# Performance work log

Measured on AMD Instinct MI355X. Metric: run time of the kernel, lower is better.

## Reference

```python
import jax, jax.numpy as jnp
import numpy as np
from jax import lax

A_NUM = 3
STRIDES = (4, 8, 16, 32, 64)
LEVEL_HW = ((128, 208), (64, 104), (32, 52), (16, 26), (8, 13))
IMG_H, IMG_W = 512.0, 832.0
PRE_NMS, POST_NMS, NMS_TH = 6000, 1000, 0.7


def _base_anchors(base_size, ratios=(0.5, 1.0, 2.0), scales=(8.0,)):
    ratios = np.asarray(ratios, np.float64)
    scales = np.asarray(scales, np.float64)
    cx = cy = (base_size - 1) / 2.0
    size = float(base_size) * float(base_size)
    ws = np.round(np.sqrt(size / ratios))
    hs = np.round(ws * ratios)
    ws = (ws[:, None] * scales[None, :]).reshape(-1)
    hs = (hs[:, None] * scales[None, :]).reshape(-1)
    return np.stack([cx - 0.5 * (ws - 1), cy - 0.5 * (hs - 1),
                     cx + 0.5 * (ws - 1), cy + 0.5 * (hs - 1)], axis=1)


def _all_anchors():
    # generate_anchors_global: per-level shifted grids, concatenated, order (h, w, a)
    out = []
    for stride, (h, w) in zip(STRIDES, LEVEL_HW):
        base = _base_anchors(stride)  # [A,4]
        sx = np.arange(w) * stride
        sy = np.arange(h) * stride
        sx, sy = np.meshgrid(sx, sy)
        shifts = np.stack([sx.ravel(), sy.ravel(), sx.ravel(), sy.ravel()], axis=1)
        anc = (shifts[:, None, :] + base[None, :, :]).reshape(-1, 4)  # [H*W*A,4]
        out.append(anc)
    return np.concatenate(out, axis=0).astype(np.float32)

_ANCHORS = _all_anchors()


def _conv(x, w, b, pad):
    y = lax.conv_general_dilated(x, w, (1, 1), [(pad, pad), (pad, pad)],
                                 dimension_numbers=('NCHW', 'OIHW', 'NCHW'))
    return y + b[None, :, None, None]


def _bbox_transform_inv(anchors, deltas):
    w = anchors[:, 2] - anchors[:, 0] + 1.0
    h = anchors[:, 3] - anchors[:, 1] + 1.0
    cx = anchors[:, 0] + 0.5 * w
    cy = anchors[:, 1] + 0.5 * h
    dx, dy, dw, dh = deltas[:, 0], deltas[:, 1], deltas[:, 2], deltas[:, 3]
    pcx = dx * w + cx
    pcy = dy * h + cy
    pw = jnp.exp(dw) * w
    ph = jnp.exp(dh) * h
    return jnp.stack([pcx - 0.5 * pw, pcy - 0.5 * ph,
                      pcx + 0.5 * pw, pcy + 0.5 * ph], axis=1)


def _iou_one_to_many(box, boxes):
    area = (boxes[:, 2] - boxes[:, 0] + 1.0) * (boxes[:, 3] - boxes[:, 1] + 1.0)
    area_b = (box[2] - box[0] + 1.0) * (box[3] - box[1] + 1.0)
    xx1 = jnp.maximum(box[0], boxes[:, 0])
    yy1 = jnp.maximum(box[1], boxes[:, 1])
    xx2 = jnp.minimum(box[2], boxes[:, 2])
    yy2 = jnp.minimum(box[3], boxes[:, 3])
    iw = jnp.maximum(0.0, xx2 - xx1 + 1.0)
    ih = jnp.maximum(0.0, yy2 - yy1 + 1.0)
    inter = iw * ih
    return inter / (area + area_b - inter)


def _nms_fixed(boxes, scores, thresh, max_out):
    # greedy NMS with a fixed number of iterations (jit-friendly)
    def body(s, _):
        i = jnp.argmax(s)
        valid = s[i] > -jnp.inf
        ious = _iou_one_to_many(boxes[i], boxes)
        s2 = jnp.where(ious > thresh, -jnp.inf, s)
        s2 = s2.at[i].set(-jnp.inf)
        return s2, (i, valid)
    _, (idx, valid) = lax.scan(body, scores, None, length=max_out)
    return idx, valid


def _rpn_forward(feats, im_info, rpn_conv_w, rpn_conv_b, rpn_score_w,
                 rpn_score_b, rpn_bbox_w, rpn_bbox_b):
    fg_scores, bbox_deltas = [], []
    for p in feats:
        H, W = p.shape[-2], p.shape[-1]
        f = _conv(p, rpn_conv_w, rpn_conv_b, 1)              # [1,512,H,W]
        cls = _conv(f, rpn_score_w, rpn_score_b, 0)          # [1,2A,H,W]
        # _reshape_layer(.,2) + softmax(dim=1) + _reshape_layer back + permute
        prob = jax.nn.softmax(cls.reshape(1, 2, A_NUM, H, W), axis=1)
        prob = prob.reshape(1, 2 * A_NUM, H, W).transpose(0, 2, 3, 1)  # [1,H,W,2A]
        fg = prob[..., A_NUM:].reshape(-1)                    # fg prob, order (h,w,a)
        bb = _conv(f, rpn_bbox_w, rpn_bbox_b, 0).transpose(0, 2, 3, 1).reshape(-1, 4)
        fg_scores.append(fg)
        bbox_deltas.append(bb)
    scores = jnp.concatenate(fg_scores, axis=0)              # [Ntot]
    deltas = jnp.concatenate(bbox_deltas, axis=0)            # [Ntot,4]
    anchors = jnp.asarray(_ANCHORS)

    proposals = _bbox_transform_inv(anchors, deltas)
    # clip to image
    proposals = jnp.stack([
        jnp.clip(proposals[:, 0], 0.0, im_info[1] - 1.0),
        jnp.clip(proposals[:, 1], 0.0, im_info[0] - 1.0),
        jnp.clip(proposals[:, 2], 0.0, im_info[1] - 1.0),
        jnp.clip(proposals[:, 3], 0.0, im_info[0] - 1.0)], axis=1)

    # pre-NMS top-k by score
    top_scores, order = lax.top_k(scores, PRE_NMS)
    top_boxes = proposals[order]
    keep, valid = _nms_fixed(top_boxes, top_scores, NMS_TH, POST_NMS)
    vmask = valid.astype(top_boxes.dtype)[:, None]
    sel_boxes = top_boxes[keep] * vmask
    sel_scores = top_scores[keep][:, None] * vmask
    rois = jnp.concatenate([jnp.zeros((POST_NMS, 1), sel_boxes.dtype), sel_boxes], axis=1)
    return jnp.concatenate([rois, sel_scores], axis=1)        # [POST_NMS, 6]


def setup_inputs() -> dict:
    key = jax.random.key(0)
    ks = jax.random.split(key, 12)
    chans = 256
    feats = {}
    for i, (name, (h, w)) in enumerate(zip(['p2', 'p3', 'p4', 'p5', 'p6'], LEVEL_HW)):
        feats[name] = jax.random.normal(ks[i], (1, chans, h, w), jnp.float32)
    inp = dict(feats)
    inp['im_info'] = jnp.array([IMG_H, IMG_W, 1.0], jnp.float32)
    inp['rpn_conv_w'] = jax.random.normal(ks[5], (512, chans, 3, 3), jnp.float32) * 0.03
    inp['rpn_conv_b'] = jnp.zeros((512,), jnp.float32)
    inp['rpn_score_w'] = jax.random.normal(ks[6], (2 * A_NUM, 512, 1, 1), jnp.float32) * 0.03
    inp['rpn_score_b'] = jnp.zeros((2 * A_NUM,), jnp.float32)
    inp['rpn_bbox_w'] = jax.random.normal(ks[7], (4 * A_NUM, 512, 1, 1), jnp.float32) * 0.01
    inp['rpn_bbox_b'] = jnp.zeros((4 * A_NUM,), jnp.float32)
    return inp


def reference(p2, p3, p4, p5, p6, im_info, rpn_conv_w, rpn_conv_b,
              rpn_score_w, rpn_score_b, rpn_bbox_w, rpn_bbox_b):
    return _rpn_forward([p2, p3, p4, p5, p6], im_info, rpn_conv_w, rpn_conv_b,
                        rpn_score_w, rpn_score_b, rpn_bbox_w, rpn_bbox_b)
```

## Files before the change

kernel.cpp:

```cpp
#include <hip/hip_runtime.h>
#include <stdint.h>

#define N_ANCH   106392
#define PRE_NMS  6000
#define POST_NMS 1000
#define POOL_CAP 8192
#define NMS_BLKS 94
#define SUP_W    96

static __device__ const int    LV_H[5]      = {128, 64, 32, 16, 8};
static __device__ const int    LV_W[5]      = {208, 104, 52, 26, 13};
static __device__ const int    LV_STRIDE[5] = {4, 8, 16, 32, 64};
static __device__ const int    LV_PIX[5]    = {26624, 6656, 1664, 416, 104};
static __device__ const int    LV_TILE0[6]  = {0, 416, 520, 546, 553, 555};
static __device__ const int    LV_AOFF[6]   = {0, 79872, 99840, 104832, 106080, 106392};
static __device__ const int    GPOFF[6]     = {0, 26624, 33280, 34944, 35360, 35464};
static __device__ const double BASE_ANCH[5][3][4] = {
  {{-22.,-10.,25.,13.},   {-14.,-14.,17.,17.},    {-10.,-22.,13.,25.}},
  {{-40.,-20.,47.,27.},   {-28.,-28.,35.,35.},    {-20.,-44.,27.,51.}},
  {{-84.,-40.,99.,55.},   {-56.,-56.,71.,71.},    {-36.,-80.,51.,95.}},
  {{-164.,-72.,195.,103.},{-112.,-112.,143.,143.},{-76.,-168.,107.,199.}},
  {{-332.,-152.,395.,215.},{-224.,-224.,287.,287.},{-148.,-328.,211.,391.}}
};

__device__ __forceinline__ uint32_t sort32f(float f) {
  uint32_t u = __float_as_uint(f);
  return ((int)u < 0) ? ~u : (u | 0x80000000u);
}
__device__ __forceinline__ uint64_t sort64(double d) {
  uint64_t u = (uint64_t)__double_as_longlong(d);
  return ((long long)u < 0) ? ~u : (u | 0x8000000000000000ull);
}

__device__ __forceinline__ double combf(const float* sw, const float* bw, int c, int j) {
  if (j < 3) return (double)sw[(3 + j) * 512 + c] - (double)sw[j * 512 + c];
  return (double)bw[(j - 3) * 512 + c];
}

__global__ __launch_bounds__(256) void k_weff_part(const float* __restrict__ cw,
                                                   const float* __restrict__ sw,
                                                   const float* __restrict__ bw,
                                                   double* __restrict__ Wpart) {
  int chunk = blockIdx.x / 9;
  int tb = blockIdx.x % 9;
  int t = tb * 256 + threadIdx.x;
  int c0 = chunk * 32;
  double acc[15];
#pragma unroll
  for (int j = 0; j < 15; ++j) acc[j] = 0.0;
#pragma unroll 1
  for (int c = c0; c < c0 + 32; ++c) {
    double v = (double)cw[c * 2304 + t];
#pragma unroll
    for (int j = 0; j < 15; ++j) acc[j] += v * combf(sw, bw, c, j);
  }
  double* o = Wpart + (((size_t)chunk * 2304 + t) << 4);
#pragma unroll
  for (int j = 0; j < 15; ++j) o[j] = acc[j];
  o[15] = 0.0;
}

__global__ __launch_bounds__(256) void k_weff_fin(const double* __restrict__ Wpart,
                                                  const float* __restrict__ cb,
                                                  const float* __restrict__ sb,
                                                  const float* __restrict__ bb,
                                                  const float* __restrict__ sw,
                                                  const float* __restrict__ bw,
                                                  double* __restrict__ Weff,
                                                  double* __restrict__ fb,
                                                  float4* __restrict__ w3,
                                                  float* __restrict__ fb32) {
  if (blockIdx.x == 9) {
    __shared__ double ps[15][16];
    int tid = threadIdx.x;
    if (tid < 240) {
      int j = tid >> 4, part = tid & 15;
      double s = 0.0;
      for (int c = part * 32; c < part * 32 + 32; ++c)
        s += (double)cb[c] * combf(sw, bw, c, j);
      ps[j][part] = s;
    }
    __syncthreads();
    if (tid < 15) {
      double s = 0.0;
#pragma unroll
      for (int part = 0; part < 16; ++part) s += ps[tid][part];
      s += (tid < 3) ? ((double)sb[3 + tid] - (double)sb[tid]) : (double)bb[tid - 3];
      fb[tid] = s;
      if (tid < 3) fb32[tid] = (float)s;
    }
    if (tid == 15) fb32[3] = 0.f;
    return;
  }
  int t = blockIdx.x * 256 + threadIdx.x;
  double acc[15];
#pragma unroll
  for (int j = 0; j < 15; ++j) acc[j] = 0.0;
#pragma unroll 1
  for (int chunk = 0; chunk < 16; ++chunk) {
    const double* p = Wpart + (((size_t)chunk * 2304 + t) << 4);
#pragma unroll
    for (int j = 0; j < 15; ++j) acc[j] += p[j];
  }
  double* o = Weff + ((size_t)t << 4);
#pragma unroll
  for (int j = 0; j < 15; ++j) o[j] = acc[j];
  o[15] = 0.0;
  float4 wf;
  wf.x = (float)acc[0]; wf.y = (float)acc[1]; wf.z = (float)acc[2]; wf.w = 0.f;
  w3[t] = wf;
}

__global__ __launch_bounds__(256) void k_w5(const double* __restrict__ Weff,
                                            double* __restrict__ w5) {
  int idx = blockIdx.x * 256 + threadIdx.x;
  if (idx >= 2304 * 3) return;
  int t = idx / 3, a = idx % 3;
  int ci = t / 9, t9 = t % 9;
  const double* src = Weff + ((size_t)t << 4);
  double* dst = w5 + (size_t)ci * 192 + (size_t)(t9 * 3 + a) * 6;
  int jd = 3 + 4 * a;
  dst[0] = src[jd + 0];
  dst[1] = src[jd + 1];
  dst[2] = src[jd + 2];
  dst[3] = src[jd + 3];
  dst[4] = src[a];
  dst[5] = 0.0;
}

__device__ __forceinline__ void load9(float v[9], const float* __restrict__ ib,
                                      const bool rok[3], const bool cok[3],
                                      const int roff[3]) {
#pragma unroll
  for (int ky = 0; ky < 3; ++ky)
#pragma unroll
    for (int kx = 0; kx < 3; ++kx)
      v[ky * 3 + kx] = (rok[ky] && cok[kx]) ? ib[roff[ky] + kx] : 0.0f;
}

__global__ __launch_bounds__(256) void k_fast(
    const float* __restrict__ p0, const float* __restrict__ p1,
    const float* __restrict__ p2, const float* __restrict__ p3,
    const float* __restrict__ p4,
    const float4* __restrict__ w3, const float* __restrict__ fb32,
    float* __restrict__ logits32, uint32_t* __restrict__ hist) {
  __shared__ float4 w3s[2304];
  __shared__ float red[4][64][3];
  int tid = threadIdx.x, wv = tid >> 6, ln = tid & 63;
  for (int i = tid; i < 2304; i += 256) w3s[i] = w3[i];
  int t = blockIdx.x;
  int L = 0;
  while (L < 4 && t >= LV_TILE0[L + 1]) ++L;
  const float* inL = (L == 0) ? p0 : (L == 1) ? p1 : (L == 2) ? p2 : (L == 3) ? p3 : p4;
  int H = LV_H[L], W = LV_W[L], HW = H * W, PIX = LV_PIX[L];
  int pix = (t - LV_TILE0[L]) * 64 + ln;
  bool valid = pix < PIX;
  if (!valid) pix = PIX - 1;
  int h = pix / W, w = pix % W;
  bool rok[3], cok[3];
  int roff[3];
#pragma unroll
  for (int ky = 0; ky < 3; ++ky) {
    int iy = h + ky - 1;
    rok[ky] = (iy >= 0 && iy < H);
    roff[ky] = iy * W + w - 1;
  }
#pragma unroll
  for (int kx = 0; kx < 3; ++kx) {
    int ix = w + kx - 1;
    cok[kx] = (ix >= 0 && ix < W);
  }
  __syncthreads();
  float a0 = 0.f, a1 = 0.f, a2 = 0.f;
  int ci0 = wv * 64;
  const float* ib = inL + ci0 * HW;
#pragma unroll 1
  for (int ci = ci0; ci < ci0 + 64; ++ci, ib += HW) {
    float v[9];
    load9(v, ib, rok, cok, roff);
    const float4* wr = w3s + ci * 9;
#pragma unroll
    for (int t9 = 0; t9 < 9; ++t9) {
      float4 wt = wr[t9];
      float vv = v[t9];
      a0 += vv * wt.x; a1 += vv * wt.y; a2 += vv * wt.z;
    }
  }
  red[wv][ln][0] = a0; red[wv][ln][1] = a1; red[wv][ln][2] = a2;
  __syncthreads();
  if (wv == 0 && valid) {
    int gbase = LV_AOFF[L] + pix * 3;
#pragma unroll
    for (int a = 0; a < 3; ++a) {
      float f = (red[0][ln][a] + red[1][ln][a]) + (red[2][ln][a] + red[3][ln][a]);
      f += fb32[a];
      logits32[gbase + a] = f;
      atomicAdd(&hist[sort32f(f) >> 16], 1u);
    }
  }
}

__global__ __launch_bounds__(1024) void k_edge(const uint32_t* __restrict__ hist,
                                               uint32_t* __restrict__ cnts) {
  __shared__ uint32_t cs[1024];
  __shared__ uint32_t g_grp, g_suf;
  int t = threadIdx.x, wv = t >> 6, ln = t & 63;
#pragma unroll 4
  for (int r = 0; r < 64; ++r) {
    int g = r * 16 + wv;
    uint32_t x = hist[g * 64 + ln];
#pragma unroll
    for (int off = 32; off > 0; off >>= 1) x += __shfl_down(x, off);
    if (ln == 0) cs[g] = x;
  }
  __syncthreads();
  for (int off = 1; off < 1024; off <<= 1) {
    uint32_t v = cs[t] + ((t + off < 1024) ? cs[t + off] : 0u);
    __syncthreads();
    cs[t] = v;
    __syncthreads();
  }
  uint32_t sufnext = (t < 1023) ? cs[t + 1] : 0u;
  if (cs[t] >= PRE_NMS && sufnext < PRE_NMS) {
    g_grp = (uint32_t)t;
    g_suf = sufnext;
  }
  __syncthreads();
  if (t < 64) {
    uint32_t grp = g_grp, suf = g_suf;
    uint32_t x = hist[grp * 64 + t];
    uint32_t S = x;
#pragma unroll
    for (int off = 1; off < 64; off <<= 1) {
      uint32_t y = __shfl_down(S, off);
      if (t + off < 64) S += y;
    }
    unsigned long long mask = __ballot(suf + S >= PRE_NMS);
    int hi = 63 - (int)__clzll(mask);
    if (t == hi) {
      uint32_t e = grp * 64 + (uint32_t)hi;
      cnts[1] = (e > 2) ? e - 2 : 0;
    }
  }
}

__global__ __launch_bounds__(256) void k_cnt(const float* __restrict__ logits32,
                                             const uint32_t* __restrict__ cnts,
                                             uint32_t* __restrict__ bcnt) {
  __shared__ uint32_t wc[4];
  int tid = threadIdx.x;
  int i = blockIdx.x * 256 + tid;
  uint32_t edge = cnts[1];
  bool pass = (i < N_ANCH) && ((sort32f(logits32[i]) >> 16) >= edge);
  unsigned long long m = __ballot(pass);
  if ((tid & 63) == 0) wc[tid >> 6] = (uint32_t)__popcll(m);
  __syncthreads();
  if (tid == 0) bcnt[blockIdx.x] = wc[0] + wc[1] + wc[2] + wc[3];
}

__global__ __launch_bounds__(256) void k_fill(const float* __restrict__ logits32,
                                              uint32_t* __restrict__ cnts,
                                              const uint32_t* __restrict__ bcnt,
                                              uint32_t* __restrict__ alist) {
  __shared__ uint32_t red[256];
  __shared__ uint32_t woff[4];
  int tid = threadIdx.x, wv = tid >> 6, ln = tid & 63;
  uint32_t s = 0;
  for (int k = tid; k < blockIdx.x; k += 256) s += bcnt[k];
  red[tid] = s;
  __syncthreads();
#pragma unroll
  for (int off = 128; off > 0; off >>= 1) {
    if (tid < off) red[tid] += red[tid + off];
    __syncthreads();
  }
  uint32_t base = red[0];
  int i = blockIdx.x * 256 + tid;
  uint32_t edge = cnts[1];
  bool pass = (i < N_ANCH) && ((sort32f(logits32[i]) >> 16) >= edge);
  unsigned long long m = __ballot(pass);
  if (ln == 0) woff[wv] = (uint32_t)__popcll(m);
  __syncthreads();
  uint32_t off_in_blk = 0;
  for (int k = 0; k < wv; ++k) off_in_blk += woff[k];
  if (pass) {
    uint32_t pos = base + off_in_blk + (uint32_t)__popcll(m & ((1ull << ln) - 1ull));
    if (pos < POOL_CAP) alist[pos] = (uint32_t)i;
  }
  if (blockIdx.x == ((N_ANCH + 255) / 256 - 1) && tid == 0)
    cnts[0] = base + woff[0] + woff[1] + woff[2] + woff[3];
}

__global__ __launch_bounds__(256) void k_refine(
    const float* __restrict__ p0, const float* __restrict__ p1,
    const float* __restrict__ p2, const float* __restrict__ p3,
    const float* __restrict__ p4,
    const double* __restrict__ w5, const double* __restrict__ fb,
    const uint32_t* __restrict__ alist, const uint32_t* __restrict__ cnts,
    double* __restrict__ logits, double* __restrict__ deltas,
    uint64_t* __restrict__ pkey) {
  __shared__ int4 wlds[4][768];
  __shared__ double red[4][64][5];
  int tid = threadIdx.x, wv = tid >> 6, ln = tid & 63;
  int cnt = (int)cnts[0];
  if (cnt > POOL_CAP) cnt = POOL_CAP;
  int base = blockIdx.x * 64;
  if (base >= cnt) return;
  int slot = base + ln;
  if (slot >= cnt) slot = cnt - 1;
  int gi = (int)alist[slot];
  int gpix = gi / 3, a = gi - gpix * 3;
  int L = 0;
  while (L < 4 && gpix >= GPOFF[L + 1]) ++L;
  int pix = gpix - GPOFF[L];
  const float* inL = (L == 0) ? p0 : (L == 1) ? p1 : (L == 2) ? p2 : (L == 3) ? p3 : p4;
  int H = LV_H[L], W = LV_W[L], HW = H * W;
  int h = pix / W, w = pix % W;
  bool rok[3], cok[3];
  int roff[3];
#pragma unroll
  for (int ky = 0; ky < 3; ++ky) {
    int iy = h + ky - 1;
    rok[ky] = (iy >= 0 && iy < H);
    roff[ky] = iy * W + w - 1;
  }
#pragma unroll
  for (int kx = 0; kx < 3; ++kx) {
    int ix = w + kx - 1;
    cok[kx] = (ix >= 0 && ix < W);
  }
  const char* wbc = (const char*)&wlds[wv][0];
  {
    const int4* gs = (const int4*)((const char*)w5 + (size_t)(wv * 64) * 1536);
    int4 r[12];
#pragma unroll
    for (int i = 0; i < 12; ++i) r[i] = gs[i * 64 + ln];
#pragma unroll
    for (int i = 0; i < 12; ++i) wlds[wv][i * 64 + ln] = r[i];
  }
  double sc = 0.0, d0 = 0.0, d1 = 0.0, d2 = 0.0, d3 = 0.0;
  const float* ibn = inL + (size_t)(wv * 64) * HW;
  float vn[9];
  load9(vn, ibn, rok, cok, roff);
#pragma unroll 1
  for (int k = 0; k < 8; ++k) {
    int4 r[12];
    if (k < 7) {
      const int4* gs =
          (const int4*)((const char*)w5 + (size_t)(wv * 64 + (k + 1) * 8) * 1536);
#pragma unroll
      for (int i = 0; i < 12; ++i) r[i] = gs[i * 64 + ln];
    }
#pragma unroll 1
    for (int c2 = 0; c2 < 8; ++c2) {
      float vc[9];
#pragma unroll
      for (int q = 0; q < 9; ++q) vc[q] = vn[q];
      int lc = k * 8 + c2;
      if (lc < 63) {
        ibn += HW;
        load9(vn, ibn, rok, cok, roff);
      }
      const char* b2 = wbc + c2 * 1536 + a * 48;
#pragma unroll
      for (int t9 = 0; t9 < 9; ++t9) {
        double vd = (double)vc[t9];
        double2 w01 = *(const double2*)(b2 + t9 * 144);
        double2 w23 = *(const double2*)(b2 + t9 * 144 + 16);
        double  w4  = *(const double*)(b2 + t9 * 144 + 32);
        d0 += vd * w01.x; d1 += vd * w01.y;
        d2 += vd * w23.x; d3 += vd * w23.y;
        sc += vd * w4;
      }
    }
    if (k < 7) {
#pragma unroll
      for (int i = 0; i < 12; ++i) wlds[wv][i * 64 + ln] = r[i];
    }
  }
  red[wv][ln][0] = sc;
  red[wv][ln][1] = d0; red[wv][ln][2] = d1;
  red[wv][ln][3] = d2; red[wv][ln][4] = d3;
  __syncthreads();
  if (wv == 0) {
    int js = a, jd = 3 + 4 * a;
    double f[5];
#pragma unroll
    for (int j = 0; j < 5; ++j)
      f[j] = red[0][ln][j] + red[1][ln][j] + red[2][ln][j] + red[3][ln][j];
    double lg = f[0] + fb[js];
    logits[gi] = lg;
    deltas[gi * 4 + 0] = f[1] + fb[jd + 0];
    deltas[gi * 4 + 1] = f[2] + fb[jd + 1];
    deltas[gi * 4 + 2] = f[3] + fb[jd + 2];
    deltas[gi * 4 + 3] = f[4] + fb[jd + 3];
    pkey[slot] = (sort64(lg) & ~0x1FFFFull) | (uint64_t)(0x1FFFFu - (uint32_t)gi);
  }
}

__global__ __launch_bounds__(256) void k_rank_cnt(const uint32_t* __restrict__ cnts,
                                                  const uint64_t* __restrict__ pkey,
                                                  uint32_t* __restrict__ rank32) {
  __shared__ uint64_t lk[512];
  int t = threadIdx.x;
  int cnt = (int)cnts[0];
  if (cnt > POOL_CAP) cnt = POOL_CAP;
  int it = blockIdx.x >> 4, jc = blockIdx.x & 15;
  int e = it * 256 + t;
  int c0 = jc * 512;
  if (it * 256 >= cnt || c0 >= cnt) return;
  int lim = cnt - c0; if (lim > 512) lim = 512;
  for (int i = t; i < 512; i += 256) lk[i] = (i < lim) ? pkey[c0 + i] : 0ull;
  __syncthreads();
  bool active = e < cnt;
  uint64_t mykey = active ? pkey[e] : ~0ull;
  int r = 0;
#pragma unroll 8
  for (int j = 0; j < 512; ++j) r += (lk[j] > mykey) ? 1 : 0;
  if (active && r) atomicAdd(&rank32[e], (uint32_t)r);
}

__global__ __launch_bounds__(256) void k_scatter(const uint32_t* __restrict__ cnts,
                                                 const uint64_t* __restrict__ pkey,
                                                 const uint32_t* __restrict__ rank32,
                                                 const double* __restrict__ logits,
                                                 const double* __restrict__ deltas,
                                                 const float* __restrict__ im_info,
                                                 double* __restrict__ ss,
                                                 double* __restrict__ sbx,
                                                 float4* __restrict__ bxf,
                                                 float* __restrict__ areaf) {
  int t = threadIdx.x;
  int cnt = (int)cnts[0];
  if (cnt > POOL_CAP) cnt = POOL_CAP;
  int e = blockIdx.x * 256 + t;
  if (blockIdx.x * 256 >= cnt) return;
  if (e >= cnt) return;
  int rank = (int)rank32[e];
  if (rank >= PRE_NMS) return;
  uint64_t mykey = pkey[e];
  int gi = 0x1FFFF - (int)(mykey & 0x1FFFFull);
  int L = 0;
  while (L < 4 && gi >= LV_AOFF[L + 1]) ++L;
  int rel = gi - LV_AOFF[L];
  int pix = rel / 3, a = rel % 3;
  int W = LV_W[L];
  int h = pix / W, w = pix % W;
  double imW1 = (double)im_info[1] - 1.0;
  double imH1 = (double)im_info[0] - 1.0;
  double shx = (double)(w * LV_STRIDE[L]), shy = (double)(h * LV_STRIDE[L]);
  double ax1 = BASE_ANCH[L][a][0] + shx, ay1 = BASE_ANCH[L][a][1] + shy;
  double ax2 = BASE_ANCH[L][a][2] + shx, ay2 = BASE_ANCH[L][a][3] + shy;
  double dx = deltas[gi * 4 + 0], dy = deltas[gi * 4 + 1];
  double dw = deltas[gi * 4 + 2], dh = deltas[gi * 4 + 3];
  double wa = ax2 - ax1 + 1.0, ha = ay2 - ay1 + 1.0;
  double cx = ax1 + 0.5 * wa, cy = ay1 + 0.5 * ha;
  double pcx = dx * wa + cx, pcy = dy * ha + cy;
  double pw = exp(dw) * wa, ph = exp(dh) * ha;
  double x1 = fmin(fmax(pcx - 0.5 * pw, 0.0), imW1);
  double y1 = fmin(fmax(pcy - 0.5 * ph, 0.0), imH1);
  double x2 = fmin(fmax(pcx + 0.5 * pw, 0.0), imW1);
  double y2 = fmin(fmax(pcy + 0.5 * ph, 0.0), imH1);
  ss[rank] = 1.0 / (1.0 + exp(-logits[gi]));
  sbx[rank * 4 + 0] = x1; sbx[rank * 4 + 1] = y1;
  sbx[rank * 4 + 2] = x2; sbx[rank * 4 + 3] = y2;
  float4 bf;
  bf.x = (float)x1; bf.y = (float)y1; bf.z = (float)x2; bf.w = (float)y2;
  bxf[rank] = bf;
  areaf[rank] = (float)((x2 - x1 + 1.0) * (y2 - y1 + 1.0));
}

__device__ __forceinline__ bool iou_gt(const double* A, const double* B) {
  double areaA = (A[2] - A[0] + 1.0) * (A[3] - A[1] + 1.0);
  double areaB = (B[2] - B[0] + 1.0) * (B[3] - B[1] + 1.0);
  double xx1 = fmax(A[0], B[0]), yy1 = fmax(A[1], B[1]);
  double xx2 = fmin(A[2], B[2]), yy2 = fmin(A[3], B[3]);
  double iw = fmax(0.0, xx2 - xx1 + 1.0), ih = fmax(0.0, yy2 - yy1 + 1.0);
  double inter = iw * ih;
  return inter > 0.7 * (areaA + areaB - inter);
}

__global__ __launch_bounds__(256) void k_build(const double* __restrict__ sbx,
                                               const float4* __restrict__ bxf,
                                               const float* __restrict__ areaf,
                                               uint64_t* __restrict__ Sup) {
  __shared__ float cbx[256][5];
  __shared__ float rbx[64][5];
  int blk = blockIdx.x;
  int rtile = blk / 24, ctile = blk % 24;
  int t = threadIdx.x, q = t >> 6, ln = t & 63;
  int r = rtile * 64 + ln;
  int w = ctile * 4 + q;
  {
    int c = ctile * 256 + t;
    float4 b;
    float ar;
    if (c < NMS_BLKS * 64) { b = bxf[c]; ar = areaf[c]; }
    else { b.x = b.y = b.z = b.w = 0.f; ar = 0.f; }
    cbx[t][0] = b.x; cbx[t][1] = b.y; cbx[t][2] = b.z; cbx[t][3] = b.w; cbx[t][4] = ar;
    if (t < 64) {
      int rr = rtile * 64 + t;
      float4 rb = bxf[rr];
      rbx[t][0] = rb.x; rbx[t][1] = rb.y; rbx[t][2] = rb.z; rbx[t][3] = rb.w;
      rbx[t][4] = areaf[rr];
    }
  }
  __syncthreads();
  uint64_t bits = 0ull;
  int j0 = w * 64;
  if (w < NMS_BLKS && j0 + 63 > r) {
    float ax1 = rbx[ln][0], ay1 = rbx[ln][1], ax2 = rbx[ln][2], ay2 = rbx[ln][3];
    float aar = rbx[ln][4];
#pragma unroll 4
    for (int jj = 0; jj < 64; ++jj) {
      int j = j0 + jj;
      if (j <= r) continue;
      int cl = q * 64 + jj;
      float iw = fminf(ax2, cbx[cl][2]) - fmaxf(ax1, cbx[cl][0]) + 1.f;
      float ih = fminf(ay2, cbx[cl][3]) - fmaxf(ay1, cbx[cl][1]) + 1.f;
      float inter = fmaxf(iw, 0.f) * fmaxf(ih, 0.f);
      float d = inter - 0.7f * (aar + cbx[cl][4] - inter);
      bool sup;
      if (d > 4.0f) sup = true;
      else if (d < -4.0f) sup = false;
      else sup = iou_gt(sbx + (size_t)r * 4, sbx + (size_t)j * 4);
      if (sup) bits |= 1ull << jj;
    }
  }
  Sup[(size_t)r * SUP_W + w] = bits;
}

__global__ __launch_bounds__(1024) void k_scan(const uint64_t* __restrict__ Sup,
                                               const double* __restrict__ ss,
                                               const double* __restrict__ sbx,
                                               float* __restrict__ out) {
  __shared__ uint16_t keep[POST_NMS];
  __shared__ uint32_t ext_arr[NMS_BLKS][2];
  __shared__ int s_kcnt;
  int t = threadIdx.x, wv = t >> 6, ln = t & 63;
  for (int i = t; i < NMS_BLKS * 2; i += 1024) ext_arr[i >> 1][i & 1] = 0u;
  if (t == 0) s_kcnt = 0;
  uint64_t nrow = 0ull;
  if (wv == 0) nrow = Sup[(size_t)ln * SUP_W];
  __syncthreads();
  for (int b = 0; b < NMS_BLKS; ++b) {
    if (wv == 0) {
      uint64_t myrow = nrow & ~((2ull << ln) - 1ull);
      if (b + 1 < NMS_BLKS)
        nrow = Sup[(size_t)((b + 1) * 64 + ln) * SUP_W + (b + 1)];
      uint64_t ext = ((uint64_t)ext_arr[b][1] << 32) | ext_arr[b][0];
      int base = b * 64;
      if (base + 63 >= PRE_NMS) {
        int v = PRE_NMS - base;
        ext |= ~((1ull << v) - 1ull);
      }
      int K0 = s_kcnt;
      uint64_t avail = ~ext;
      uint64_t kp = 0ull;
      int lim = POST_NMS - K0, nk = 0;
      while (avail && nk < lim) {
        int i2 = __ffsll((unsigned long long)avail) - 1;
        kp |= 1ull << i2;
        ++nk;
        uint64_t row = __shfl(myrow, i2);
        avail &= ~row;
        avail &= ~(1ull << i2);
      }
      if ((kp >> ln) & 1ull) {
        int pos = K0 + __popcll(kp & ((1ull << ln) - 1ull));
        keep[pos] = (uint16_t)(base + ln);
      }
      if (ln == 0) s_kcnt = K0 + nk;
    }
    __syncthreads();
    int K = s_kcnt;
    if (K >= POST_NMS || b + 1 >= NMS_BLKS) break;
    uint64_t m = 0ull;
    for (int p = t; p < K; p += 1024) m |= Sup[(size_t)keep[p] * SUP_W + (b + 1)];
#pragma unroll
    for (int off = 32; off > 0; off >>= 1) m |= __shfl_down(m, off);
    if (ln == 0 && m) {
      uint32_t lo = (uint32_t)m, hi = (uint32_t)(m >> 32);
      if (lo) atomicOr(&ext_arr[b + 1][0], lo);
      if (hi) atomicOr(&ext_arr[b + 1][1], hi);
    }
    __syncthreads();
  }
  __syncthreads();
  int KF = s_kcnt;
  for (int r = t; r < POST_NMS; r += 1024) {
    float* o = out + r * 6;
    if (r < KF) {
      int p = keep[r];
      o[0] = 0.f;
      o[1] = (float)sbx[p * 4 + 0];
      o[2] = (float)sbx[p * 4 + 1];
      o[3] = (float)sbx[p * 4 + 2];
      o[4] = (float)sbx[p * 4 + 3];
      o[5] = (float)ss[p];
    } else {
#pragma unroll
      for (int c = 0; c < 6; ++c) o[c] = 0.f;
    }
  }
}

extern "C" void kernel_launch(void* const* d_in, const int* in_sizes, int n_in,
                              void* d_out, int out_size, void* d_ws, size_t ws_size,
                              hipStream_t stream) {
  const float* p0 = (const float*)d_in[0];
  const float* p1 = (const float*)d_in[1];
  const float* p2 = (const float*)d_in[2];
  const float* p3 = (const float*)d_in[3];
  const float* p4 = (const float*)d_in[4];
  const float* im_info = (const float*)d_in[5];
  const float* cw = (const float*)d_in[6];
  const float* cb = (const float*)d_in[7];
  const float* sw = (const float*)d_in[8];
  const float* sb = (const float*)d_in[9];
  const float* bw = (const float*)d_in[10];
  const float* bb = (const float*)d_in[11];
  char* ws = (char*)d_ws;
  uint32_t* hist    = (uint32_t*)(ws + 0);
  uint32_t* cnts    = (uint32_t*)(ws + 262144);
  double*   fb      = (double*)  (ws + 262208);
  float*    fb32    = (float*)   (ws + 262336);
  double*   logits  = (double*)  (ws + 262352);
  double*   deltas  = (double*)  (ws + 1113488);
  float*    logits32= (float*)   (ws + 4518032);
  float4*   w3      = (float4*)  (ws + 4943600);
  double*   Weff    = (double*)  (ws + 4980464);
  double*   Wpart   = (double*)  (ws + 5275376);
  uint32_t* alist   = (uint32_t*)(ws + 9993968);
  double*   ssort   = (double*)  (ws + 10026736);
  double*   sbx     = (double*)  (ws + 10074864);
  float4*   bxf     = (float4*)  (ws + 10267376);
  float*    areaf   = (float*)   (ws + 10363632);
  uint64_t* Sup     = (uint64_t*)(ws + 10387696);
  uint64_t* pkey    = (uint64_t*)(ws + 15007984);
  uint32_t* rank32  = (uint32_t*)(ws + 15073520);
  uint32_t* bcnt    = hist;
  double*   W5      = Wpart;
  float* out = (float*)d_out;

  hipMemsetAsync(ws, 0, 262208, stream);
  hipMemsetAsync(rank32, 0, 32768, stream);
  k_weff_part<<<144, 256, 0, stream>>>(cw, sw, bw, Wpart);
  k_weff_fin<<<10, 256, 0, stream>>>(Wpart, cb, sb, bb, sw, bw, Weff, fb, w3, fb32);
  k_w5<<<27, 256, 0, stream>>>(Weff, W5);
  k_fast<<<555, 256, 0, stream>>>(p0, p1, p2, p3, p4, w3, fb32, logits32, hist);
  k_edge<<<1, 1024, 0, stream>>>(hist, cnts);
  k_cnt<<<416, 256, 0, stream>>>(logits32, cnts, bcnt);
  k_fill<<<416, 256, 0, stream>>>(logits32, cnts, bcnt, alist);
  k_refine<<<128, 256, 0, stream>>>(p0, p1, p2, p3, p4, W5, fb, alist, cnts,
                                    logits, deltas, pkey);
  k_rank_cnt<<<512, 256, 0, stream>>>(cnts, pkey, rank32);
  k_scatter<<<32, 256, 0, stream>>>(cnts, pkey, rank32, logits, deltas, im_info,
                                    ssort, sbx, bxf, areaf);
  k_build<<<94 * 24, 256, 0, stream>>>(sbx, bxf, areaf, Sup);
  k_scan<<<1, 1024, 0, stream>>>(Sup, ssort, sbx, out);
}
```

Before: 461.4 us.

## Process four 64-box NMS blocks per scan phase to cut barriers

The serial NMS scan kernel now handles 256 candidates per phase, four 64-bit blocks, instead of one 64-box block per iteration. Wave 0 holds the intra-phase suppression-mask tiles in registers and does greedy selection across the four blocks with shuffles. Kept boxes then OR their masks into the next four blocks' external-suppression words. This cuts the number of block-wide barriers and global passes over kept rows by about four times. The cost is more register pressure and some wasted work on the padded tail rows.

```diff
diff --git a/kernel.cpp b/kernel.cpp
--- a/kernel.cpp
+++ b/kernel.cpp
@@ -7,6 +7,7 @@
 #define POOL_CAP 8192
 #define NMS_BLKS 94
 #define SUP_W    96
+#define NPH      24
 
 static __device__ const int    LV_H[5]      = {128, 64, 32, 16, 8};
 static __device__ const int    LV_W[5]      = {208, 104, 52, 26, 13};
@@ -535,54 +536,125 @@
                                                const double* __restrict__ sbx,
                                                float* __restrict__ out) {
   __shared__ uint16_t keep[POST_NMS];
-  __shared__ uint32_t ext_arr[NMS_BLKS][2];
+  __shared__ uint32_t ext_arr[SUP_W][2];
   __shared__ int s_kcnt;
   int t = threadIdx.x, wv = t >> 6, ln = t & 63;
-  for (int i = t; i < NMS_BLKS * 2; i += 1024) ext_arr[i >> 1][i & 1] = 0u;
+  for (int i = t; i < SUP_W * 2; i += 1024) ext_arr[i >> 1][i & 1] = 0u;
   if (t == 0) s_kcnt = 0;
-  uint64_t nrow = 0ull;
-  if (wv == 0) nrow = Sup[(size_t)ln * SUP_W];
-  __syncthreads();
-  for (int b = 0; b < NMS_BLKS; ++b) {
+  const int RMAX = NMS_BLKS * 64 - 1;
+  uint64_t m00 = 0, m01 = 0, m02 = 0, m03 = 0;
+  uint64_t m11 = 0, m12 = 0, m13 = 0;
+  uint64_t m22 = 0, m23 = 0;
+  uint64_t m33 = 0;
+  if (wv == 0) {
+    size_t r0 = (size_t)ln * SUP_W;
+    size_t r1 = (size_t)(64 + ln) * SUP_W;
+    size_t r2 = (size_t)(128 + ln) * SUP_W;
+    size_t r3 = (size_t)(192 + ln) * SUP_W;
+    m00 = Sup[r0 + 0]; m01 = Sup[r0 + 1]; m02 = Sup[r0 + 2]; m03 = Sup[r0 + 3];
+    m11 = Sup[r1 + 1]; m12 = Sup[r1 + 2]; m13 = Sup[r1 + 3];
+    m22 = Sup[r2 + 2]; m23 = Sup[r2 + 3];
+    m33 = Sup[r3 + 3];
+  }
+  __syncthreads();
+  for (int p = 0; p < NPH; ++p) {
     if (wv == 0) {
-      uint64_t myrow = nrow & ~((2ull << ln) - 1ull);
-      if (b + 1 < NMS_BLKS)
-        nrow = Sup[(size_t)((b + 1) * 64 + ln) * SUP_W + (b + 1)];
-      uint64_t ext = ((uint64_t)ext_arr[b][1] << 32) | ext_arr[b][0];
-      int base = b * 64;
-      if (base + 63 >= PRE_NMS) {
-        int v = PRE_NMS - base;
-        ext |= ~((1ull << v) - 1ull);
+      int wb = 4 * p, base = 256 * p;
+      uint64_t dmask = ~((2ull << ln) - 1ull);
+      uint64_t d00 = m00 & dmask, d11 = m11 & dmask;
+      uint64_t d22 = m22 & dmask, d33 = m33 & dmask;
+      uint64_t a0, a1, a2, a3;
+      {
+        uint64_t e0 = ((uint64_t)ext_arr[wb + 0][1] << 32) | ext_arr[wb + 0][0];
+        uint64_t e1 = ((uint64_t)ext_arr[wb + 1][1] << 32) | ext_arr[wb + 1][0];
+        uint64_t e2 = ((uint64_t)ext_arr[wb + 2][1] << 32) | ext_arr[wb + 2][0];
+        uint64_t e3 = ((uint64_t)ext_arr[wb + 3][1] << 32) | ext_arr[wb + 3][0];
+        int v0 = PRE_NMS - (base + 0),   v1 = PRE_NMS - (base + 64);
+        int v2 = PRE_NMS - (base + 128), v3 = PRE_NMS - (base + 192);
+        uint64_t t0 = (v0 >= 64) ? 0ull : ((v0 <= 0) ? ~0ull : ~((1ull << v0) - 1ull));
+        uint64_t t1 = (v1 >= 64) ? 0ull : ((v1 <= 0) ? ~0ull : ~((1ull << v1) - 1ull));
+        uint64_t t2 = (v2 >= 64) ? 0ull : ((v2 <= 0) ? ~0ull : ~((1ull << v2) - 1ull));
+        uint64_t t3 = (v3 >= 64) ? 0ull : ((v3 <= 0) ? ~0ull : ~((1ull << v3) - 1ull));
+        a0 = ~(e0 | t0); a1 = ~(e1 | t1); a2 = ~(e2 | t2); a3 = ~(e3 | t3);
       }
       int K0 = s_kcnt;
-      uint64_t avail = ~ext;
-      uint64_t kp = 0ull;
       int lim = POST_NMS - K0, nk = 0;
-      while (avail && nk < lim) {
-        int i2 = __ffsll((unsigned long long)avail) - 1;
-        kp |= 1ull << i2;
-        ++nk;
-        uint64_t row = __shfl(myrow, i2);
-        avail &= ~row;
-        avail &= ~(1ull << i2);
+      uint64_t kp0 = 0, kp1 = 0, kp2 = 0, kp3 = 0;
+      while ((a0 | a1 | a2 | a3) && nk < lim) {
+        if (a0) {
+          int i = __ffsll((unsigned long long)a0) - 1;
+          kp0 |= 1ull << i; ++nk;
+          a0 &= ~__shfl(d00, i) & ~(1ull << i);
+          a1 &= ~__shfl(m01, i);
+          a2 &= ~__shfl(m02, i);
+          a3 &= ~__shfl(m03, i);
+        } else if (a1) {
+          int i = __ffsll((unsigned long long)a1) - 1;
+          kp1 |= 1ull << i; ++nk;
+          a1 &= ~__shfl(d11, i) & ~(1ull << i);
+          a2 &= ~__shfl(m12, i);
+          a3 &= ~__shfl(m13, i);
+        } else if (a2) {
+          int i = __ffsll((unsigned long long)a2) - 1;
+          kp2 |= 1ull << i; ++nk;
+          a2 &= ~__shfl(d22, i) & ~(1ull << i);
+          a3 &= ~__shfl(m23, i);
+        } else {
+          int i = __ffsll((unsigned long long)a3) - 1;
+          kp3 |= 1ull << i; ++nk;
+          a3 &= ~__shfl(d33, i) & ~(1ull << i);
+        }
       }
-      if ((kp >> ln) & 1ull) {
-        int pos = K0 + __popcll(kp & ((1ull << ln) - 1ull));
-        keep[pos] = (uint16_t)(base + ln);
+      uint64_t below = (1ull << ln) - 1ull;
+      int c0 = __popcll(kp0), c1 = __popcll(kp1), c2 = __popcll(kp2);
+      if ((kp0 >> ln) & 1ull)
+        keep[K0 + __popcll(kp0 & below)] = (uint16_t)(base + ln);
+      if ((kp1 >> ln) & 1ull)
+        keep[K0 + c0 + __popcll(kp1 & below)] = (uint16_t)(base + 64 + ln);
+      if ((kp2 >> ln) & 1ull)
+        keep[K0 + c0 + c1 + __popcll(kp2 & below)] = (uint16_t)(base + 128 + ln);
+      if ((kp3 >> ln) & 1ull)
+        keep[K0 + c0 + c1 + c2 + __popcll(kp3 & below)] = (uint16_t)(base + 192 + ln);
+      if (ln == 0) s_kcnt = K0 + nk;
+      if (p + 1 < NPH) {
+        int nb = 4 * (p + 1), rb = 256 * (p + 1);
+        int i0 = rb + ln, i1 = rb + 64 + ln, i2 = rb + 128 + ln, i3 = rb + 192 + ln;
+        size_t r0 = (size_t)(i0 > RMAX ? RMAX : i0) * SUP_W;
+        size_t r1 = (size_t)(i1 > RMAX ? RMAX : i1) * SUP_W;
+        size_t r2 = (size_t)(i2 > RMAX ? RMAX : i2) * SUP_W;
+        size_t r3 = (size_t)(i3 > RMAX ? RMAX : i3) * SUP_W;
+        m00 = Sup[r0 + nb + 0]; m01 = Sup[r0 + nb + 1];
+        m02 = Sup[r0 + nb + 2]; m03 = Sup[r0 + nb + 3];
+        m11 = Sup[r1 + nb + 1]; m12 = Sup[r1 + nb + 2]; m13 = Sup[r1 + nb + 3];
+        m22 = Sup[r2 + nb + 2]; m23 = Sup[r2 + nb + 3];
+        m33 = Sup[r3 + nb + 3];
       }
-      if (ln == 0) s_kcnt = K0 + nk;
     }
     __syncthreads();
     int K = s_kcnt;
-    if (K >= POST_NMS || b + 1 >= NMS_BLKS) break;
-    uint64_t m = 0ull;
-    for (int p = t; p < K; p += 1024) m |= Sup[(size_t)keep[p] * SUP_W + (b + 1)];
-#pragma unroll
-    for (int off = 32; off > 0; off >>= 1) m |= __shfl_down(m, off);
-    if (ln == 0 && m) {
-      uint32_t lo = (uint32_t)m, hi = (uint32_t)(m >> 32);
-      if (lo) atomicOr(&ext_arr[b + 1][0], lo);
-      if (hi) atomicOr(&ext_arr[b + 1][1], hi);
+    if (K >= POST_NMS || p + 1 >= NPH) break;
+    int nb = 4 * (p + 1);
+    uint64_t o0 = 0, o1 = 0, o2 = 0, o3 = 0;
+    for (int q = t; q < K; q += 1024) {
+      const uint64_t* Sr = Sup + (size_t)keep[q] * SUP_W + nb;
+      o0 |= Sr[0]; o1 |= Sr[1]; o2 |= Sr[2]; o3 |= Sr[3];
+    }
+#pragma unroll
+    for (int off = 32; off > 0; off >>= 1) {
+      o0 |= __shfl_down(o0, off);
+      o1 |= __shfl_down(o1, off);
+      o2 |= __shfl_down(o2, off);
+      o3 |= __shfl_down(o3, off);
+    }
+    if (ln == 0) {
+      if ((uint32_t)o0)         atomicOr(&ext_arr[nb + 0][0], (uint32_t)o0);
+      if ((uint32_t)(o0 >> 32)) atomicOr(&ext_arr[nb + 0][1], (uint32_t)(o0 >> 32));
+      if ((uint32_t)o1)         atomicOr(&ext_arr[nb + 1][0], (uint32_t)o1);
+      if ((uint32_t)(o1 >> 32)) atomicOr(&ext_arr[nb + 1][1], (uint32_t)(o1 >> 32));
+      if ((uint32_t)o2)         atomicOr(&ext_arr[nb + 2][0], (uint32_t)o2);
+      if ((uint32_t)(o2 >> 32)) atomicOr(&ext_arr[nb + 2][1], (uint32_t)(o2 >> 32));
+      if ((uint32_t)o3)         atomicOr(&ext_arr[nb + 3][0], (uint32_t)o3);
+      if ((uint32_t)(o3 >> 32)) atomicOr(&ext_arr[nb + 3][1], (uint32_t)(o3 >> 32));
     }
     __syncthreads();
   }
```

New measurement: 543.9 us. +17.9%, slower.

## Overlap NMS suppression propagation with serial block scan in k_scan

Applied to the files above, without the earlier changes.

Restructures the serial NMS scan so that wave 0 decides keeps for block b and directly ORs the next block's suppression mask from the newly kept rows. Meanwhile the other 15 waves incrementally propagate suppression from the previously kept rows into all later column blocks. This replaces the per-block full re-scan of all kept rows and removes one barrier per iteration. The cost is more atomics on shared memory and a more intricate deferred update scheme whose correctness depends on the one-block lag.

```diff
diff --git a/kernel.cpp b/kernel.cpp
--- a/kernel.cpp
+++ b/kernel.cpp
@@ -535,19 +535,29 @@
                                                const double* __restrict__ sbx,
                                                float* __restrict__ out) {
   __shared__ uint16_t keep[POST_NMS];
-  __shared__ uint32_t ext_arr[NMS_BLKS][2];
-  __shared__ int s_kcnt;
+  __shared__ uint32_t ext_arr[SUP_W][2];
+  __shared__ int s_kcnt, s_done;
+  __shared__ int s_pend[2][2];
   int t = threadIdx.x, wv = t >> 6, ln = t & 63;
-  for (int i = t; i < NMS_BLKS * 2; i += 1024) ext_arr[i >> 1][i & 1] = 0u;
-  if (t == 0) s_kcnt = 0;
-  uint64_t nrow = 0ull;
-  if (wv == 0) nrow = Sup[(size_t)ln * SUP_W];
+  for (int i = t; i < SUP_W * 2; i += 1024) ext_arr[i >> 1][i & 1] = 0u;
+  if (t == 0) { s_kcnt = 0; s_done = 0; }
+  if (t < 4) s_pend[t >> 1][t & 1] = 0;
+  uint64_t diag = 0ull, nxt = 0ull;
+  if (wv == 0) {
+    size_t r = (size_t)ln * SUP_W;
+    diag = Sup[r + 0];
+    nxt  = Sup[r + 1];
+  }
   __syncthreads();
   for (int b = 0; b < NMS_BLKS; ++b) {
     if (wv == 0) {
-      uint64_t myrow = nrow & ~((2ull << ln) - 1ull);
-      if (b + 1 < NMS_BLKS)
-        nrow = Sup[(size_t)((b + 1) * 64 + ln) * SUP_W + (b + 1)];
+      uint64_t myrow = diag & ~((2ull << ln) - 1ull);
+      uint64_t mynxt = nxt;
+      if (b + 1 < NMS_BLKS) {
+        size_t r = (size_t)((b + 1) * 64 + ln) * SUP_W;
+        diag = Sup[r + (b + 1)];
+        nxt  = Sup[r + (b + 2)];
+      }
       uint64_t ext = ((uint64_t)ext_arr[b][1] << 32) | ext_arr[b][0];
       int base = b * 64;
       if (base + 63 >= PRE_NMS) {
@@ -570,21 +580,35 @@
         int pos = K0 + __popcll(kp & ((1ull << ln) - 1ull));
         keep[pos] = (uint16_t)(base + ln);
       }
-      if (ln == 0) s_kcnt = K0 + nk;
+      uint64_t v = ((kp >> ln) & 1ull) ? mynxt : 0ull;
+#pragma unroll
+      for (int off = 32; off > 0; off >>= 1) v |= __shfl_down(v, off);
+      if (ln == 0) {
+        if ((uint32_t)v)         atomicOr(&ext_arr[b + 1][0], (uint32_t)v);
+        if ((uint32_t)(v >> 32)) atomicOr(&ext_arr[b + 1][1], (uint32_t)(v >> 32));
+        s_kcnt = K0 + nk;
+        s_pend[(b + 1) & 1][0] = K0;
+        s_pend[(b + 1) & 1][1] = K0 + nk;
+        if (K0 + nk >= POST_NMS || b + 1 >= NMS_BLKS) s_done = 1;
+      }
+    } else {
+      int lo = s_pend[b & 1][0], hi = s_pend[b & 1][1];
+      if (hi > lo) {
+        int tt = t - 64;
+        int g = tt / 96, w = tt - g * 96;
+        if (w >= b + 1) {
+          uint64_t v = 0ull;
+          for (int q = lo + g; q < hi; q += 10)
+            v |= Sup[(size_t)keep[q] * SUP_W + w];
+          if (v) {
+            if ((uint32_t)v)         atomicOr(&ext_arr[w][0], (uint32_t)v);
+            if ((uint32_t)(v >> 32)) atomicOr(&ext_arr[w][1], (uint32_t)(v >> 32));
+          }
+        }
+      }
     }
     __syncthreads();
-    int K = s_kcnt;
-    if (K >= POST_NMS || b + 1 >= NMS_BLKS) break;
-    uint64_t m = 0ull;
-    for (int p = t; p < K; p += 1024) m |= Sup[(size_t)keep[p] * SUP_W + (b + 1)];
-#pragma unroll
-    for (int off = 32; off > 0; off >>= 1) m |= __shfl_down(m, off);
-    if (ln == 0 && m) {
-      uint32_t lo = (uint32_t)m, hi = (uint32_t)(m >> 32);
-      if (lo) atomicOr(&ext_arr[b + 1][0], lo);
-      if (hi) atomicOr(&ext_arr[b + 1][1], hi);
-    }
-    __syncthreads();
+    if (s_done) break;
   }
   __syncthreads();
   int KF = s_kcnt;
```

After: 458.2 us. Within noise of the previous version (-0.7%).
